# Optimization experiments

Measured on AMD Instinct MI355X. Metric: run time of the kernel, lower is better.

## Reference

```python
import jax, jax.numpy as jnp
import numpy as np

N_QUBITS = 12
K_STEPS = 6
VOCAB = 32000
D_EMB = 512
N_CLASSES = 8
B = 256
SEQ = 128
DIM = 2 ** N_QUBITS


def apply_1q(psi, U, q):
    # psi: [B, 2^n]; U: [2,2] (shared) or [B,2,2] (per-sample). Apply on wire q
    # (PennyLane convention: wire 0 = most significant axis).
    b = psi.shape[0]
    left, right = 2 ** q, 2 ** (N_QUBITS - q - 1)
    st = psi.reshape(b, left, 2, right)
    if U.ndim == 3:
        st = jnp.einsum('bij,bajr->bair', U, st)
    else:
        st = jnp.einsum('ij,bajr->bair', U, st)
    return st.reshape(b, DIM)


def apply_cnot(psi, c, t):
    b = psi.shape[0]
    st = psi.reshape((b,) + (2,) * N_QUBITS)
    c_ax, t_ax = 1 + c, 1 + t
    c0 = jnp.take(st, 0, axis=c_ax)
    c1 = jnp.take(st, 1, axis=c_ax)
    t_ax2 = t_ax - 1 if t_ax > c_ax else t_ax  # axis shift after take
    c1 = jnp.flip(c1, axis=t_ax2)
    return jnp.stack([c0, c1], axis=c_ax).reshape(b, DIM)


def ry_mat(angle):
    # angle: [B] -> [B,2,2] complex64
    c = jnp.cos(angle / 2)
    s = jnp.sin(angle / 2)
    row0 = jnp.stack([c, -s], axis=-1)
    row1 = jnp.stack([s, c], axis=-1)
    return jnp.stack([row0, row1], axis=-2).astype(jnp.complex64)


def rot_mat(phi, theta, omega):
    # PennyLane Rot(phi, theta, omega) = RZ(omega) RY(theta) RZ(phi)
    c = jnp.cos(theta / 2)
    s = jnp.sin(theta / 2)
    ep = jnp.exp(-0.5j * (phi + omega).astype(jnp.complex64))
    em = jnp.exp(0.5j * (phi - omega).astype(jnp.complex64))
    m = jnp.stack([jnp.stack([ep * c, -em * s]), jnp.stack([jnp.conj(em) * s, jnp.conj(ep) * c])])
    return m.astype(jnp.complex64)


def block(psi, x, theta_k):
    # data reupload RY(x_i), trainable Rot, ring of CNOTs (noiseless)
    for i in range(N_QUBITS):
        psi = apply_1q(psi, ry_mat(x[:, i]), i)
    for i in range(N_QUBITS):
        psi = apply_1q(psi, rot_mat(theta_k[i, 0], theta_k[i, 1], theta_k[i, 2]), i)
    for i in range(N_QUBITS - 1):
        psi = apply_cnot(psi, i, i + 1)
    psi = apply_cnot(psi, N_QUBITS - 1, 0)
    return psi


def z_expvals(psi):
    # <Z_i> for all wires from |psi|^2
    b = psi.shape[0]
    p = (psi.real ** 2 + psi.imag ** 2).reshape((b,) + (2,) * N_QUBITS)
    zs = []
    for i in range(N_QUBITS):
        axes = tuple(ax for ax in range(1, N_QUBITS + 1) if ax != 1 + i)
        m = p.sum(axis=axes)  # [B,2]
        zs.append(m[:, 0] - m[:, 1])
    return jnp.stack(zs, axis=-1)  # [B, n_qubits]


def _forward(input_ids, attention_mask, emb_table, proj_w, proj_b, theta, head_w, head_b):
    # encoder: embed -> masked mean pool -> tanh(linear) * pi
    e = emb_table[input_ids]                              # [B,S,D]
    mask = attention_mask[:, :, None].astype(jnp.float32)
    pooled = (e * mask).sum(axis=1) / jnp.clip(mask.sum(axis=1), 1.0)
    x = jnp.tanh(pooled @ proj_w.T + proj_b) * jnp.float32(np.pi)  # [B, n_qubits]

    b = x.shape[0]
    psi = jnp.zeros((b, DIM), jnp.complex64).at[:, 0].set(1.0)
    readouts = []
    for k in range(K_STEPS):
        psi = block(psi, x, theta[k])
        readouts.append(z_expvals(psi))
    step_readouts = jnp.stack(readouts, axis=0)           # [K,B,n_qubits]
    step_logits = step_readouts @ head_w.T + head_b       # [K,B,n_classes]
    return step_logits, step_readouts, step_logits[-1]


def setup_inputs() -> dict:
    key = jax.random.key(0)
    ks = jax.random.split(key, 6)
    input_ids = jax.random.randint(ks[0], (B, SEQ), 0, VOCAB)
    attention_mask = jnp.ones((B, SEQ), dtype=jnp.int32)
    emb_table = jax.random.normal(ks[1], (VOCAB, D_EMB), jnp.float32)
    emb_table = emb_table.at[0].set(0.0)  # padding_idx=0 row is zeros
    proj_w = jax.random.normal(ks[2], (N_QUBITS, D_EMB), jnp.float32) / np.sqrt(D_EMB)
    proj_b = jnp.zeros((N_QUBITS,), jnp.float32)
    theta = 0.01 * jax.random.normal(ks[3], (K_STEPS, N_QUBITS, 3), jnp.float32)
    head_w = jax.random.normal(ks[4], (N_CLASSES, N_QUBITS), jnp.float32) / np.sqrt(N_QUBITS)
    head_b = jnp.zeros((N_CLASSES,), jnp.float32)
    return {'input_ids': input_ids, 'attention_mask': attention_mask,
            'emb_table': emb_table, 'proj_w': proj_w, 'proj_b': proj_b,
            'theta': theta, 'head_w': head_w, 'head_b': head_b}


def reference(input_ids, attention_mask, emb_table, proj_w, proj_b, theta, head_w, head_b):
    return _forward(input_ids, attention_mask, emb_table, proj_w, proj_b, theta, head_w, head_b)
```

## Files before the change

### kernel.cpp

```cpp
#include <hip/hip_runtime.h>
#include <math.h>

#define NQ 12
#define DIM 4096
#define KS 6
#define BB 256
#define SEQ 128
#define DEMB 512


#define REG_GATE(P, W) { \
    const float* u = &s_u[k][W][0]; \
    float u00r=u[0],u00i=u[1],u01r=u[2],u01i=u[3]; \
    float u10r=u[4],u10i=u[5],u11r=u[6],u11i=u[7]; \
    _Pragma("unroll") \
    for (int r0 = 0; r0 < 8; ++r0) if (!(r0 & (1 << (P)))) { \
        int r1 = r0 | (1 << (P)); \
        float2 A = a[r0], Bv = a[r1]; \
        a[r0].x = u00r*A.x - u00i*A.y + u01r*Bv.x - u01i*Bv.y; \
        a[r0].y = u00r*A.y + u00i*A.x + u01r*Bv.y + u01i*Bv.x; \
        a[r1].x = u10r*A.x - u10i*A.y + u11r*Bv.x - u11i*Bv.y; \
        a[r1].y = u10r*A.y + u10i*A.x + u11r*Bv.y + u11i*Bv.x; \
    } }

#define BF_PLAIN(v, m) { float p_ = __shfl_xor(v, m, 64); v = v + p_; }
#define BF_SIGN(v, m)  { float p_ = __shfl_xor(v, m, 64); float d_ = v - p_; \
                         v = (lane & m) ? -d_ : d_; }

__global__ __launch_bounds__(512) void fused_kernel(
    const int* __restrict__ ids, const int* __restrict__ mask,
    const float* __restrict__ emb, const float* __restrict__ pw,
    const float* __restrict__ pb, const float* __restrict__ theta,
    const float* __restrict__ hw, const float* __restrict__ hb,
    float* __restrict__ readouts, float* __restrict__ logits,
    float* __restrict__ last)
{
    __shared__ float2 buf0[DIM];
    __shared__ float2 buf1[DIM];
    __shared__ float  s_u[KS][NQ][8];
    __shared__ float  s_red[8][NQ];
    __shared__ float  s_msum[4];
    __shared__ float  s_wred[2][NQ];
    __shared__ float  s_x[NQ];
    __shared__ float  s_hw[8 * NQ];
    __shared__ float  s_hb[8];

    int b = blockIdx.x;
    int tid = threadIdx.x;
    int lane = tid & 63, wave = tid >> 6;

    int*    s_ids = (int*)buf1;
    float*  s_m   = (float*)buf1 + SEQ;
    float4* s_part = (float4*)buf0;

    if (tid < SEQ) {
        s_ids[tid] = ids[b * SEQ + tid];
        s_m[tid]   = (float)mask[b * SEQ + tid];
    }
    if (tid >= 256 && tid < 256 + 8 * NQ) s_hw[tid - 256] = hw[tid - 256];
    if (tid >= 384 && tid < 392)          s_hb[tid - 384] = hb[tid - 384];
    __syncthreads();

    {
        int g = tid >> 7, e = tid & 127;
        float4 acc = make_float4(0.f, 0.f, 0.f, 0.f);
        float msum = 0.f;
        #pragma unroll 4
        for (int s = g; s < SEQ; s += 4) {
            float m = s_m[s];
            float4 v = ((const float4*)emb)[(size_t)s_ids[s] * 128 + e];
            acc.x = fmaf(m, v.x, acc.x);
            acc.y = fmaf(m, v.y, acc.y);
            acc.z = fmaf(m, v.z, acc.z);
            acc.w = fmaf(m, v.w, acc.w);
            msum += m;
        }
        __syncthreads();
        s_part[g * 128 + e] = acc;
        if (e == 0) s_msum[g] = msum;
    }
    __syncthreads();

    if (tid < 128) {
        float tm = fmaxf(s_msum[0] + s_msum[1] + s_msum[2] + s_msum[3], 1.f);
        float inv = 1.f / tm;
        float4 p0 = s_part[0 * 128 + tid], p1 = s_part[1 * 128 + tid];
        float4 p2 = s_part[2 * 128 + tid], p3 = s_part[3 * 128 + tid];
        float4 p;
        p.x = (p0.x + p1.x + p2.x + p3.x) * inv;
        p.y = (p0.y + p1.y + p2.y + p3.y) * inv;
        p.z = (p0.z + p1.z + p2.z + p3.z) * inv;
        p.w = (p0.w + p1.w + p2.w + p3.w) * inv;
        float z[NQ];
        #pragma unroll
        for (int i = 0; i < NQ; ++i) {
            float4 w4 = ((const float4*)pw)[i * 128 + tid];
            z[i] = p.x * w4.x + p.y * w4.y + p.z * w4.z + p.w * w4.w;
        }
        #pragma unroll
        for (int i = 0; i < NQ; ++i) {
            #pragma unroll
            for (int off = 32; off > 0; off >>= 1)
                z[i] += __shfl_xor(z[i], off, 64);
        }
        if ((tid & 63) == 0) {
            int w = tid >> 6;
            #pragma unroll
            for (int i = 0; i < NQ; ++i) s_wred[w][i] = z[i];
        }
    }
    __syncthreads();
    if (tid < NQ) {
        float d = pb[tid] + s_wred[0][tid] + s_wred[1][tid];
        s_x[tid] = tanhf(d) * 3.14159274101257324f;
    }
    __syncthreads();

    if (tid < KS * NQ) {
        int k = tid / NQ, w = tid % NQ;
        float ang = s_x[w];
        float cy = cosf(0.5f * ang), sy = sinf(0.5f * ang);
        const float* th = theta + (k * NQ + w) * 3;
        float phi = th[0], te = th[1], om = th[2];
        float ct = cosf(0.5f * te), st = sinf(0.5f * te);
        float a1 = -0.5f * (phi + om);
        float epr = cosf(a1), epi = sinf(a1);
        float a2 = 0.5f * (phi - om);
        float emr = cosf(a2), emi = sinf(a2);
        float R00r = epr * ct,  R00i = epi * ct;
        float R01r = -emr * st, R01i = -emi * st;
        float R10r = emr * st,  R10i = -emi * st;
        float R11r = epr * ct,  R11i = -epi * ct;
        s_u[k][w][0] =  R00r * cy + R01r * sy;
        s_u[k][w][1] =  R00i * cy + R01i * sy;
        s_u[k][w][2] = -R00r * sy + R01r * cy;
        s_u[k][w][3] = -R00i * sy + R01i * cy;
        s_u[k][w][4] =  R10r * cy + R11r * sy;
        s_u[k][w][5] =  R10i * cy + R11i * sy;
        s_u[k][w][6] = -R10r * sy + R11r * cy;
        s_u[k][w][7] = -R10i * sy + R11i * cy;
    }

    int baseWA = (tid << 3) ^ ((tid >> 1) & 15);
    int baseRB = ((lane << 3) | wave) ^ ((lane >> 1) & 15);
    int idxP[8];
    #pragma unroll
    for (int rb = 0; rb < 8; ++rb) {
        int jp = (rb << 9) | (lane << 3) | wave;
        int b0 = (jp >> 11) & 1;
        int pref = b0, outv = 0;
        for (int w = 1; w < NQ; ++w) {
            pref ^= (jp >> (11 - w)) & 1;
            outv |= pref << (11 - w);
        }
        outv |= (b0 ^ pref) << 11;
        idxP[rb] = outv ^ ((outv >> 4) & 15);
    }
    int wv2 = (wave >> 2) & 1, wv21 = ((wave >> 2) ^ (wave >> 1)) & 1;
    int wvp = ((wave >> 2) ^ (wave >> 1) ^ wave) & 1;

    float2 a[8];
    #pragma unroll
    for (int r = 0; r < 8; ++r) a[r] = make_float2(0.f, 0.f);
    if (tid == 0) a[0].x = 1.f;
    __syncthreads();

    for (int k = 0; k < KS; ++k) {
        REG_GATE(0, 11)
        REG_GATE(1, 10)
        REG_GATE(2, 9)

        #pragma unroll
        for (int p = 3; p <= 8; ++p) {
            const float* u = &s_u[k][11 - p][0];
            int q = p - 3, mk = 1 << q;
            int bit = (lane >> q) & 1;
            float c0r = bit ? u[6] : u[0];
            float c0i = bit ? u[7] : u[1];
            float c1r = bit ? u[4] : u[2];
            float c1i = bit ? u[5] : u[3];
            #pragma unroll
            for (int r = 0; r < 8; ++r) {
                float px = __shfl_xor(a[r].x, mk, 64);
                float py = __shfl_xor(a[r].y, mk, 64);
                float nx = c0r * a[r].x - c0i * a[r].y + c1r * px - c1i * py;
                float ny = c0r * a[r].y + c0i * a[r].x + c1r * py + c1i * px;
                a[r].x = nx; a[r].y = ny;
            }
        }

        #pragma unroll
        for (int r = 0; r < 8; ++r) buf0[baseWA ^ r] = a[r];
        __syncthreads();
        #pragma unroll
        for (int rb = 0; rb < 8; ++rb) a[rb] = buf0[(rb << 9) | baseRB];

        REG_GATE(0, 2)
        REG_GATE(1, 1)
        REG_GATE(2, 0)

        float pr[8];
        #pragma unroll
        for (int r = 0; r < 8; ++r)
            pr[r] = a[r].x * a[r].x + a[r].y * a[r].y;
        float r1 = (pr[0] + pr[1] + pr[6] + pr[7]) - (pr[2] + pr[3] + pr[4] + pr[5]);
        float D  = (pr[0] + pr[3] + pr[5] + pr[6]) - (pr[1] + pr[2] + pr[4] + pr[7]);
        float D0 = (pr[0] + pr[3] + pr[4] + pr[7]) - (pr[1] + pr[2] + pr[5] + pr[6]);
        float r2 = D, r3 = D, r4 = D, r5 = D, r6 = D, r7 = D, r8 = D, r0 = D0;
        BF_PLAIN(r1,32) BF_PLAIN(r2,32) BF_SIGN(r3,32) BF_SIGN(r4,32)
        BF_SIGN(r5,32)  BF_SIGN(r6,32)  BF_SIGN(r7,32) BF_SIGN(r8,32) BF_SIGN(r0,32)
        BF_PLAIN(r1,16) BF_PLAIN(r2,16) BF_PLAIN(r3,16) BF_SIGN(r4,16)
        BF_SIGN(r5,16)  BF_SIGN(r6,16)  BF_SIGN(r7,16) BF_SIGN(r8,16) BF_SIGN(r0,16)
        BF_PLAIN(r1,8)  BF_PLAIN(r2,8)  BF_PLAIN(r3,8) BF_PLAIN(r4,8)
        BF_SIGN(r5,8)   BF_SIGN(r6,8)   BF_SIGN(r7,8)  BF_SIGN(r8,8)  BF_SIGN(r0,8)
        BF_PLAIN(r1,4)  BF_PLAIN(r2,4)  BF_PLAIN(r3,4) BF_PLAIN(r4,4)
        BF_PLAIN(r5,4)  BF_SIGN(r6,4)   BF_SIGN(r7,4)  BF_SIGN(r8,4)  BF_SIGN(r0,4)
        BF_PLAIN(r1,2)  BF_PLAIN(r2,2)  BF_PLAIN(r3,2) BF_PLAIN(r4,2)
        BF_PLAIN(r5,2)  BF_PLAIN(r6,2)  BF_SIGN(r7,2)  BF_SIGN(r8,2)  BF_SIGN(r0,2)
        BF_PLAIN(r1,1)  BF_PLAIN(r2,1)  BF_PLAIN(r3,1) BF_PLAIN(r4,1)
        BF_PLAIN(r5,1)  BF_PLAIN(r6,1)  BF_PLAIN(r7,1) BF_SIGN(r8,1)  BF_SIGN(r0,1)
        if (lane == 0) {
            float* sr = s_red[wave];
            sr[0]  = wvp  ? -r0 : r0;
            sr[1]  = r1;  sr[2] = r2;  sr[3] = r3;  sr[4] = r4;
            sr[5]  = r5;  sr[6] = r6;  sr[7] = r7;  sr[8] = r8;
            sr[9]  = wv2  ? -r8 : r8;
            sr[10] = wv21 ? -r8 : r8;
            sr[11] = wvp  ? -r8 : r8;
        }

        #pragma unroll
        for (int rb = 0; rb < 8; ++rb) buf1[idxP[rb]] = a[rb];
        __syncthreads();
        #pragma unroll
        for (int r = 0; r < 8; ++r) a[r] = buf1[baseWA ^ r];

        if (tid < NQ) {
            float s = 0.f;
            #pragma unroll
            for (int w2 = 0; w2 < 8; ++w2) s += s_red[w2][tid];
            readouts[(k * BB + b) * NQ + tid] = s;
        }
        if (tid < 8) {
            float acc2 = s_hb[tid];
            #pragma unroll
            for (int i = 0; i < NQ; ++i) {
                float si = 0.f;
                #pragma unroll
                for (int w2 = 0; w2 < 8; ++w2) si += s_red[w2][i];
                acc2 = fmaf(si, s_hw[tid * NQ + i], acc2);
            }
            logits[(k * BB + b) * 8 + tid] = acc2;
            if (k == KS - 1) last[b * 8 + tid] = acc2;
        }
    }
}

extern "C" void kernel_launch(void* const* d_in, const int* in_sizes, int n_in,
                              void* d_out, int out_size, void* d_ws, size_t ws_size,
                              hipStream_t stream) {
    const int*   ids   = (const int*)d_in[0];
    const int*   mask  = (const int*)d_in[1];
    const float* emb   = (const float*)d_in[2];
    const float* pw    = (const float*)d_in[3];
    const float* pb    = (const float*)d_in[4];
    const float* theta = (const float*)d_in[5];
    const float* hw    = (const float*)d_in[6];
    const float* hb    = (const float*)d_in[7];
    float* out = (float*)d_out;

    float* readouts = out + KS * BB * 8;
    float* last     = out + KS * BB * 8 + KS * BB * NQ;

    fused_kernel<<<BB, 512, 0, stream>>>(ids, mask, emb, pw, pb, theta,
                                         hw, hb, readouts, out, last);
}
```

Measured before the change: 141.7 us.

## Double threads per block to 1024 with four amplitudes per thread

Each block now runs 1024 threads that each hold 4 complex amplitudes instead of 8, and the qubit-to-register/lane/wave mapping, LDS transpose indices, CNOT permutation and Z-expectation butterfly reductions are rederived for 16 waves. The embedding gather is split across 8 sequence groups, with partial sums stored in both shared buffers. The aim is more parallelism and less register pressure per thread for the 256 blocks. In exchange there are more shuffle-based gates, a 16-way cross-wave reduction, and barriers now span more waves.

Measured after the change: 153.1 us. +8.0%, slower.

```diff
diff --git a/kernel.cpp b/kernel.cpp
--- a/kernel.cpp
+++ b/kernel.cpp
@@ -14,7 +14,7 @@
     float u00r=u[0],u00i=u[1],u01r=u[2],u01i=u[3]; \
     float u10r=u[4],u10i=u[5],u11r=u[6],u11i=u[7]; \
     _Pragma("unroll") \
-    for (int r0 = 0; r0 < 8; ++r0) if (!(r0 & (1 << (P)))) { \
+    for (int r0 = 0; r0 < 4; ++r0) if (!(r0 & (1 << (P)))) { \
         int r1 = r0 | (1 << (P)); \
         float2 A = a[r0], Bv = a[r1]; \
         a[r0].x = u00r*A.x - u00i*A.y + u01r*Bv.x - u01i*Bv.y; \
@@ -27,7 +27,7 @@
 #define BF_SIGN(v, m)  { float p_ = __shfl_xor(v, m, 64); float d_ = v - p_; \
                          v = (lane & m) ? -d_ : d_; }
 
-__global__ __launch_bounds__(512) void fused_kernel(
+__global__ __launch_bounds__(1024) void fused_kernel(
     const int* __restrict__ ids, const int* __restrict__ mask,
     const float* __restrict__ emb, const float* __restrict__ pw,
     const float* __restrict__ pb, const float* __restrict__ theta,
@@ -38,8 +38,8 @@
     __shared__ float2 buf0[DIM];
     __shared__ float2 buf1[DIM];
     __shared__ float  s_u[KS][NQ][8];
-    __shared__ float  s_red[8][NQ];
-    __shared__ float  s_msum[4];
+    __shared__ float  s_red[16][NQ];
+    __shared__ float  s_msum[8];
     __shared__ float  s_wred[2][NQ];
     __shared__ float  s_x[NQ];
     __shared__ float  s_hw[8 * NQ];
@@ -49,9 +49,8 @@
     int tid = threadIdx.x;
     int lane = tid & 63, wave = tid >> 6;
 
-    int*    s_ids = (int*)buf1;
-    float*  s_m   = (float*)buf1 + SEQ;
-    float4* s_part = (float4*)buf0;
+    int*   s_ids = (int*)buf1;
+    float* s_m   = (float*)buf1 + SEQ;
 
     if (tid < SEQ) {
         s_ids[tid] = ids[b * SEQ + tid];
@@ -66,7 +65,7 @@
         float4 acc = make_float4(0.f, 0.f, 0.f, 0.f);
         float msum = 0.f;
         #pragma unroll 4
-        for (int s = g; s < SEQ; s += 4) {
+        for (int s = g; s < SEQ; s += 8) {
             float m = s_m[s];
             float4 v = ((const float4*)emb)[(size_t)s_ids[s] * 128 + e];
             acc.x = fmaf(m, v.x, acc.x);
@@ -76,21 +75,26 @@
             msum += m;
         }
         __syncthreads();
-        s_part[g * 128 + e] = acc;
+        float4* part = (g & 4) ? (float4*)buf1 : (float4*)buf0;
+        part[(g & 3) * 128 + e] = acc;
         if (e == 0) s_msum[g] = msum;
     }
     __syncthreads();
 
     if (tid < 128) {
-        float tm = fmaxf(s_msum[0] + s_msum[1] + s_msum[2] + s_msum[3], 1.f);
-        float inv = 1.f / tm;
-        float4 p0 = s_part[0 * 128 + tid], p1 = s_part[1 * 128 + tid];
-        float4 p2 = s_part[2 * 128 + tid], p3 = s_part[3 * 128 + tid];
-        float4 p;
-        p.x = (p0.x + p1.x + p2.x + p3.x) * inv;
-        p.y = (p0.y + p1.y + p2.y + p3.y) * inv;
-        p.z = (p0.z + p1.z + p2.z + p3.z) * inv;
-        p.w = (p0.w + p1.w + p2.w + p3.w) * inv;
+        float tm = 0.f;
+        #pragma unroll
+        for (int i = 0; i < 8; ++i) tm += s_msum[i];
+        float inv = 1.f / fmaxf(tm, 1.f);
+        float4 p = make_float4(0.f, 0.f, 0.f, 0.f);
+        #pragma unroll
+        for (int i = 0; i < 4; ++i) {
+            float4 q0 = ((float4*)buf0)[i * 128 + tid];
+            float4 q1 = ((float4*)buf1)[i * 128 + tid];
+            p.x += q0.x + q1.x; p.y += q0.y + q1.y;
+            p.z += q0.z + q1.z; p.w += q0.w + q1.w;
+        }
+        p.x *= inv; p.y *= inv; p.z *= inv; p.w *= inv;
         float z[NQ];
         #pragma unroll
         for (int i = 0; i < NQ; ++i) {
@@ -141,12 +145,14 @@
         s_u[k][w][7] = -R10i * sy + R11i * cy;
     }
 
-    int baseWA = (tid << 3) ^ ((tid >> 1) & 15);
-    int baseRB = ((lane << 3) | wave) ^ ((lane >> 1) & 15);
-    int idxP[8];
+    int baseWA = (tid << 2) ^ ((tid >> 2) & 15);
+    int jB0 = ((lane & 3) << 10) | (((lane >> 2) & 15) << 2)
+            | ((wave & 3) << 6) | ((wave >> 2) & 3);
+    int baseRB = jB0 ^ (((lane >> 4) & 3) | ((wave & 3) << 2));
+    int idxP[4];
     #pragma unroll
-    for (int rb = 0; rb < 8; ++rb) {
-        int jp = (rb << 9) | (lane << 3) | wave;
+    for (int rq = 0; rq < 4; ++rq) {
+        int jp = jB0 | (rq << 8);
         int b0 = (jp >> 11) & 1;
         int pref = b0, outv = 0;
         for (int w = 1; w < NQ; ++w) {
@@ -154,33 +160,33 @@
             outv |= pref << (11 - w);
         }
         outv |= (b0 ^ pref) << 11;
-        idxP[rb] = outv ^ ((outv >> 4) & 15);
-    }
-    int wv2 = (wave >> 2) & 1, wv21 = ((wave >> 2) ^ (wave >> 1)) & 1;
-    int wvp = ((wave >> 2) ^ (wave >> 1) ^ wave) & 1;
-
-    float2 a[8];
+        idxP[rq] = outv ^ ((outv >> 4) & 15);
+    }
+    int w0b = wave & 1, w1b = (wave >> 1) & 1;
+    int w2b = (wave >> 2) & 1, w3b = (wave >> 3) & 1;
+    int sW = w0b ^ w1b;
+
+    float2 a[4];
     #pragma unroll
-    for (int r = 0; r < 8; ++r) a[r] = make_float2(0.f, 0.f);
+    for (int r = 0; r < 4; ++r) a[r] = make_float2(0.f, 0.f);
     if (tid == 0) a[0].x = 1.f;
     __syncthreads();
 
     for (int k = 0; k < KS; ++k) {
         REG_GATE(0, 11)
         REG_GATE(1, 10)
-        REG_GATE(2, 9)
-
-        #pragma unroll
-        for (int p = 3; p <= 8; ++p) {
-            const float* u = &s_u[k][11 - p][0];
-            int q = p - 3, mk = 1 << q;
+
+        #pragma unroll
+        for (int q = 0; q < 6; ++q) {
+            const float* u = &s_u[k][9 - q][0];
+            int mk = 1 << q;
             int bit = (lane >> q) & 1;
             float c0r = bit ? u[6] : u[0];
             float c0i = bit ? u[7] : u[1];
             float c1r = bit ? u[4] : u[2];
             float c1i = bit ? u[5] : u[3];
             #pragma unroll
-            for (int r = 0; r < 8; ++r) {
+            for (int r = 0; r < 4; ++r) {
                 float px = __shfl_xor(a[r].x, mk, 64);
                 float py = __shfl_xor(a[r].y, mk, 64);
                 float nx = c0r * a[r].x - c0i * a[r].y + c1r * px - c1i * py;
@@ -190,55 +196,80 @@
         }
 
         #pragma unroll
-        for (int r = 0; r < 8; ++r) buf0[baseWA ^ r] = a[r];
+        for (int r = 0; r < 4; ++r) buf0[baseWA ^ r] = a[r];
         __syncthreads();
         #pragma unroll
-        for (int rb = 0; rb < 8; ++rb) a[rb] = buf0[(rb << 9) | baseRB];
-
-        REG_GATE(0, 2)
-        REG_GATE(1, 1)
-        REG_GATE(2, 0)
-
-        float pr[8];
-        #pragma unroll
-        for (int r = 0; r < 8; ++r)
-            pr[r] = a[r].x * a[r].x + a[r].y * a[r].y;
-        float r1 = (pr[0] + pr[1] + pr[6] + pr[7]) - (pr[2] + pr[3] + pr[4] + pr[5]);
-        float D  = (pr[0] + pr[3] + pr[5] + pr[6]) - (pr[1] + pr[2] + pr[4] + pr[7]);
-        float D0 = (pr[0] + pr[3] + pr[4] + pr[7]) - (pr[1] + pr[2] + pr[5] + pr[6]);
-        float r2 = D, r3 = D, r4 = D, r5 = D, r6 = D, r7 = D, r8 = D, r0 = D0;
-        BF_PLAIN(r1,32) BF_PLAIN(r2,32) BF_SIGN(r3,32) BF_SIGN(r4,32)
-        BF_SIGN(r5,32)  BF_SIGN(r6,32)  BF_SIGN(r7,32) BF_SIGN(r8,32) BF_SIGN(r0,32)
-        BF_PLAIN(r1,16) BF_PLAIN(r2,16) BF_PLAIN(r3,16) BF_SIGN(r4,16)
-        BF_SIGN(r5,16)  BF_SIGN(r6,16)  BF_SIGN(r7,16) BF_SIGN(r8,16) BF_SIGN(r0,16)
-        BF_PLAIN(r1,8)  BF_PLAIN(r2,8)  BF_PLAIN(r3,8) BF_PLAIN(r4,8)
-        BF_SIGN(r5,8)   BF_SIGN(r6,8)   BF_SIGN(r7,8)  BF_SIGN(r8,8)  BF_SIGN(r0,8)
-        BF_PLAIN(r1,4)  BF_PLAIN(r2,4)  BF_PLAIN(r3,4) BF_PLAIN(r4,4)
-        BF_PLAIN(r5,4)  BF_SIGN(r6,4)   BF_SIGN(r7,4)  BF_SIGN(r8,4)  BF_SIGN(r0,4)
-        BF_PLAIN(r1,2)  BF_PLAIN(r2,2)  BF_PLAIN(r3,2) BF_PLAIN(r4,2)
-        BF_PLAIN(r5,2)  BF_PLAIN(r6,2)  BF_SIGN(r7,2)  BF_SIGN(r8,2)  BF_SIGN(r0,2)
-        BF_PLAIN(r1,1)  BF_PLAIN(r2,1)  BF_PLAIN(r3,1) BF_PLAIN(r4,1)
-        BF_PLAIN(r5,1)  BF_PLAIN(r6,1)  BF_PLAIN(r7,1) BF_SIGN(r8,1)  BF_SIGN(r0,1)
+        for (int rq = 0; rq < 4; ++rq) a[rq] = buf0[baseRB | (rq << 8)];
+
+        REG_GATE(0, 3)
+        REG_GATE(1, 2)
+
+        #pragma unroll
+        for (int q = 0; q < 2; ++q) {
+            const float* u = &s_u[k][1 - q][0];
+            int mk = 1 << q;
+            int bit = (lane >> q) & 1;
+            float c0r = bit ? u[6] : u[0];
+            float c0i = bit ? u[7] : u[1];
+            float c1r = bit ? u[4] : u[2];
+            float c1i = bit ? u[5] : u[3];
+            #pragma unroll
+            for (int r = 0; r < 4; ++r) {
+                float px = __shfl_xor(a[r].x, mk, 64);
+                float py = __shfl_xor(a[r].y, mk, 64);
+                float nx = c0r * a[r].x - c0i * a[r].y + c1r * px - c1i * py;
+                float ny = c0r * a[r].y + c0i * a[r].x + c1r * py + c1i * px;
+                a[r].x = nx; a[r].y = ny;
+            }
+        }
+
+        float pr0 = a[0].x*a[0].x + a[0].y*a[0].y;
+        float pr1 = a[1].x*a[1].x + a[1].y*a[1].y;
+        float pr2 = a[2].x*a[2].x + a[2].y*a[2].y;
+        float pr3 = a[3].x*a[3].x + a[3].y*a[3].y;
+        float T   = pr0 + pr1 + pr2 + pr3;
+        float P9  = (pr0 + pr1) - (pr2 + pr3);
+        float P98 = (pr0 + pr3) - (pr1 + pr2);
+        float v1 = T, v2 = P9, v3 = P98;
+        float v6 = P98, v7 = P98, v8 = P98, v9 = P98, v0 = P98;
+        BF_PLAIN(v1,32) BF_PLAIN(v2,32) BF_PLAIN(v3,32) BF_SIGN(v6,32)
+        BF_SIGN(v7,32)  BF_SIGN(v8,32)  BF_SIGN(v9,32)  BF_SIGN(v0,32)
+        BF_PLAIN(v1,16) BF_PLAIN(v2,16) BF_PLAIN(v3,16) BF_PLAIN(v6,16)
+        BF_SIGN(v7,16)  BF_SIGN(v8,16)  BF_SIGN(v9,16)  BF_SIGN(v0,16)
+        BF_PLAIN(v1,8)  BF_PLAIN(v2,8)  BF_PLAIN(v3,8)  BF_PLAIN(v6,8)
+        BF_PLAIN(v7,8)  BF_SIGN(v8,8)   BF_SIGN(v9,8)   BF_SIGN(v0,8)
+        BF_PLAIN(v1,4)  BF_PLAIN(v2,4)  BF_PLAIN(v3,4)  BF_PLAIN(v6,4)
+        BF_PLAIN(v7,4)  BF_PLAIN(v8,4)  BF_SIGN(v9,4)   BF_SIGN(v0,4)
+        BF_SIGN(v1,2)   BF_SIGN(v2,2)   BF_SIGN(v3,2)   BF_SIGN(v6,2)
+        BF_SIGN(v7,2)   BF_SIGN(v8,2)   BF_SIGN(v9,2)   BF_PLAIN(v0,2)
+        BF_SIGN(v1,1)   BF_SIGN(v2,1)   BF_SIGN(v3,1)   BF_SIGN(v6,1)
+        BF_SIGN(v7,1)   BF_SIGN(v8,1)   BF_SIGN(v9,1)   BF_SIGN(v0,1)
         if (lane == 0) {
             float* sr = s_red[wave];
-            sr[0]  = wvp  ? -r0 : r0;
-            sr[1]  = r1;  sr[2] = r2;  sr[3] = r3;  sr[4] = r4;
-            sr[5]  = r5;  sr[6] = r6;  sr[7] = r7;  sr[8] = r8;
-            sr[9]  = wv2  ? -r8 : r8;
-            sr[10] = wv21 ? -r8 : r8;
-            sr[11] = wvp  ? -r8 : r8;
-        }
-
-        #pragma unroll
-        for (int rb = 0; rb < 8; ++rb) buf1[idxP[rb]] = a[rb];
+            sr[0]  = ((w0b^w1b^w2b^w3b) ? -v0 : v0);
+            sr[1]  = v1;
+            sr[2]  = v2;
+            sr[3]  = v3;
+            sr[4]  = w1b ? -v3 : v3;
+            sr[5]  = sW  ? -v3 : v3;
+            sr[6]  = sW  ? -v6 : v6;
+            sr[7]  = sW  ? -v7 : v7;
+            sr[8]  = sW  ? -v8 : v8;
+            sr[9]  = sW  ? -v9 : v9;
+            sr[10] = ((sW^w3b) ? -v9 : v9);
+            sr[11] = ((sW^w3b^w2b) ? -v9 : v9);
+        }
+
+        #pragma unroll
+        for (int rq = 0; rq < 4; ++rq) buf1[idxP[rq]] = a[rq];
         __syncthreads();
         #pragma unroll
-        for (int r = 0; r < 8; ++r) a[r] = buf1[baseWA ^ r];
+        for (int r = 0; r < 4; ++r) a[r] = buf1[baseWA ^ r];
 
         if (tid < NQ) {
             float s = 0.f;
             #pragma unroll
-            for (int w2 = 0; w2 < 8; ++w2) s += s_red[w2][tid];
+            for (int w2 = 0; w2 < 16; ++w2) s += s_red[w2][tid];
             readouts[(k * BB + b) * NQ + tid] = s;
         }
         if (tid < 8) {
@@ -247,7 +278,7 @@
             for (int i = 0; i < NQ; ++i) {
                 float si = 0.f;
                 #pragma unroll
-                for (int w2 = 0; w2 < 8; ++w2) si += s_red[w2][i];
+                for (int w2 = 0; w2 < 16; ++w2) si += s_red[w2][i];
                 acc2 = fmaf(si, s_hw[tid * NQ + i], acc2);
             }
             logits[(k * BB + b) * 8 + tid] = acc2;
@@ -272,6 +303,6 @@
     float* readouts = out + KS * BB * 8;
     float* last     = out + KS * BB * 8 + KS * BB * NQ;
 
-    fused_kernel<<<BB, 512, 0, stream>>>(ids, mask, emb, pw, pb, theta,
-                                         hw, hb, readouts, out, last);
+    fused_kernel<<<BB, 1024, 0, stream>>>(ids, mask, emb, pw, pb, theta,
+                                          hw, hb, readouts, out, last);
 }
```

## Replace shuffle-based middle gates with LDS transposes and restructure Z reduction

Applied to the files above, without the earlier changes.

The six middle-wire gates per step were applied with cross-lane shuffles, two per amplitude per gate. They now go through two extra shared-memory transposes, so every gate acts on register-resident pairs. The swizzle is changed to allow float4 stores and loads on the contiguous transpose, and the Z-expectation butterfly is rebuilt as a cascade that shares partial sums. This trades many shuffles for two extra barriers and more LDS traffic per step.

Measured after the change: 140.2 us. No clear change (-1.1%).

```diff
diff --git a/kernel.cpp b/kernel.cpp
--- a/kernel.cpp
+++ b/kernel.cpp
@@ -27,6 +27,8 @@
 #define BF_SIGN(v, m)  { float p_ = __shfl_xor(v, m, 64); float d_ = v - p_; \
                          v = (lane & m) ? -d_ : d_; }
 
+__device__ __forceinline__ int swz14(int x) { return x ^ ((x >> 4) & 14); }
+
 __global__ __launch_bounds__(512) void fused_kernel(
     const int* __restrict__ ids, const int* __restrict__ mask,
     const float* __restrict__ emb, const float* __restrict__ pw,
@@ -35,8 +37,8 @@
     float* __restrict__ readouts, float* __restrict__ logits,
     float* __restrict__ last)
 {
-    __shared__ float2 buf0[DIM];
-    __shared__ float2 buf1[DIM];
+    __shared__ __align__(16) float2 buf0[DIM];
+    __shared__ __align__(16) float2 buf1[DIM];
     __shared__ float  s_u[KS][NQ][8];
     __shared__ float  s_red[8][NQ];
     __shared__ float  s_msum[4];
@@ -49,8 +51,8 @@
     int tid = threadIdx.x;
     int lane = tid & 63, wave = tid >> 6;
 
-    int*    s_ids = (int*)buf1;
-    float*  s_m   = (float*)buf1 + SEQ;
+    int*   s_ids = (int*)buf1;
+    float* s_m   = (float*)buf1 + SEQ;
     float4* s_part = (float4*)buf0;
 
     if (tid < SEQ) {
@@ -141,23 +143,27 @@
         s_u[k][w][7] = -R10i * sy + R11i * cy;
     }
 
-    int baseWA = (tid << 3) ^ ((tid >> 1) & 15);
-    int baseRB = ((lane << 3) | wave) ^ ((lane >> 1) & 15);
-    int idxP[8];
+    int T8 = tid << 3;
+    int baseA  = swz14(T8);
+    int baseA4 = baseA >> 1;
+    int addrB[8], addrC[8], addrD[8], idxP[8];
     #pragma unroll
-    for (int rb = 0; rb < 8; ++rb) {
-        int jp = (rb << 9) | (lane << 3) | wave;
-        int b0 = (jp >> 11) & 1;
+    for (int r = 0; r < 8; ++r) {
+        addrB[r] = swz14((lane & 7) + 8 * r + 64 * (lane >> 3) + 512 * wave);
+        addrC[r] = swz14(lane + 64 * r + 512 * wave);
+        int jD   = lane + 64 * wave + 512 * r;
+        addrD[r] = swz14(jD);
+        int b0 = (jD >> 11) & 1;
         int pref = b0, outv = 0;
         for (int w = 1; w < NQ; ++w) {
-            pref ^= (jp >> (11 - w)) & 1;
+            pref ^= (jD >> (11 - w)) & 1;
             outv |= pref << (11 - w);
         }
         outv |= (b0 ^ pref) << 11;
-        idxP[rb] = outv ^ ((outv >> 4) & 15);
-    }
-    int wv2 = (wave >> 2) & 1, wv21 = ((wave >> 2) ^ (wave >> 1)) & 1;
-    int wvp = ((wave >> 2) ^ (wave >> 1) ^ wave) & 1;
+        idxP[r] = swz14(outv);
+    }
+    int w0b = wave & 1, w1b = (wave >> 1) & 1, w2b = (wave >> 2) & 1;
+    int wall = w0b ^ w1b ^ w2b;
 
     float2 a[8];
     #pragma unroll
@@ -166,74 +172,89 @@
     __syncthreads();
 
     for (int k = 0; k < KS; ++k) {
-        REG_GATE(0, 11)
-        REG_GATE(1, 10)
-        REG_GATE(2, 9)
-
-        #pragma unroll
-        for (int p = 3; p <= 8; ++p) {
-            const float* u = &s_u[k][11 - p][0];
-            int q = p - 3, mk = 1 << q;
-            int bit = (lane >> q) & 1;
-            float c0r = bit ? u[6] : u[0];
-            float c0i = bit ? u[7] : u[1];
-            float c1r = bit ? u[4] : u[2];
-            float c1i = bit ? u[5] : u[3];
-            #pragma unroll
-            for (int r = 0; r < 8; ++r) {
-                float px = __shfl_xor(a[r].x, mk, 64);
-                float py = __shfl_xor(a[r].y, mk, 64);
-                float nx = c0r * a[r].x - c0i * a[r].y + c1r * px - c1i * py;
-                float ny = c0r * a[r].y + c0i * a[r].x + c1r * py + c1i * px;
-                a[r].x = nx; a[r].y = ny;
+        REG_GATE(0, 11) REG_GATE(1, 10) REG_GATE(2, 9)
+
+        #pragma unroll
+        for (int i = 0; i < 4; ++i)
+            ((float4*)buf0)[baseA4 ^ i] =
+                make_float4(a[2*i].x, a[2*i].y, a[2*i+1].x, a[2*i+1].y);
+        __syncthreads();
+        #pragma unroll
+        for (int r = 0; r < 8; ++r) a[r] = buf0[addrB[r]];
+
+        REG_GATE(0, 8) REG_GATE(1, 7) REG_GATE(2, 6)
+
+        #pragma unroll
+        for (int r = 0; r < 8; ++r) buf1[addrB[r]] = a[r];
+        __syncthreads();
+        #pragma unroll
+        for (int r = 0; r < 8; ++r) a[r] = buf1[addrC[r]];
+
+        REG_GATE(0, 5) REG_GATE(1, 4) REG_GATE(2, 3)
+
+        #pragma unroll
+        for (int r = 0; r < 8; ++r) buf0[addrC[r]] = a[r];
+        __syncthreads();
+        #pragma unroll
+        for (int r = 0; r < 8; ++r) a[r] = buf0[addrD[r]];
+
+        REG_GATE(0, 2) REG_GATE(1, 1) REG_GATE(2, 0)
+
+        {
+            float p[8];
+            #pragma unroll
+            for (int r = 0; r < 8; ++r)
+                p[r] = a[r].x * a[r].x + a[r].y * a[r].y;
+            float Q1 = (p[0]+p[1]+p[6]+p[7]) - (p[2]+p[3]+p[4]+p[5]);
+            float Q2 = (p[0]+p[3]+p[5]+p[6]) - (p[1]+p[2]+p[4]+p[7]);
+            float Q0 = (p[0]+p[3]+p[4]+p[7]) - (p[1]+p[2]+p[5]+p[6]);
+            float q1 = Q1, q2p = Q2, q0 = Q0;
+            BF_PLAIN(q1,32) BF_PLAIN(q1,16) BF_PLAIN(q1,8)
+            BF_PLAIN(q1,4)  BF_PLAIN(q1,2)  BF_PLAIN(q1,1)
+            BF_PLAIN(q2p,32) BF_PLAIN(q2p,16) BF_PLAIN(q2p,8)
+            BF_PLAIN(q2p,4)  BF_PLAIN(q2p,2)  BF_PLAIN(q2p,1)
+            BF_SIGN(q0,32) BF_SIGN(q0,16) BF_SIGN(q0,8)
+            BF_SIGN(q0,4)  BF_SIGN(q0,2)  BF_SIGN(q0,1)
+            float c = Q2;
+            BF_SIGN(c,32);
+            float w6v = c; BF_PLAIN(w6v,16) BF_PLAIN(w6v,8) BF_PLAIN(w6v,4)
+                           BF_PLAIN(w6v,2)  BF_PLAIN(w6v,1)
+            BF_SIGN(c,16);
+            float w7v = c; BF_PLAIN(w7v,8) BF_PLAIN(w7v,4)
+                           BF_PLAIN(w7v,2) BF_PLAIN(w7v,1)
+            BF_SIGN(c,8);
+            float w8v = c; BF_PLAIN(w8v,4) BF_PLAIN(w8v,2) BF_PLAIN(w8v,1)
+            BF_SIGN(c,4);
+            float w9v = c; BF_PLAIN(w9v,2) BF_PLAIN(w9v,1)
+            BF_SIGN(c,2);
+            float w10v = c; BF_PLAIN(w10v,1)
+            BF_SIGN(c,1);
+            if (lane == 0) {
+                float* sr = s_red[wave];
+                sr[0]  = wall ? -q0  : q0;
+                sr[1]  = q1;
+                sr[2]  = q2p;
+                sr[3]  = w2b ? -q2p : q2p;
+                sr[4]  = (w1b ^ w2b) ? -q2p : q2p;
+                sr[5]  = wall ? -q2p : q2p;
+                sr[6]  = wall ? -w6v : w6v;
+                sr[7]  = wall ? -w7v : w7v;
+                sr[8]  = wall ? -w8v : w8v;
+                sr[9]  = wall ? -w9v : w9v;
+                sr[10] = wall ? -w10v : w10v;
+                sr[11] = wall ? -c   : c;
             }
         }
 
         #pragma unroll
-        for (int r = 0; r < 8; ++r) buf0[baseWA ^ r] = a[r];
-        __syncthreads();
-        #pragma unroll
-        for (int rb = 0; rb < 8; ++rb) a[rb] = buf0[(rb << 9) | baseRB];
-
-        REG_GATE(0, 2)
-        REG_GATE(1, 1)
-        REG_GATE(2, 0)
-
-        float pr[8];
-        #pragma unroll
-        for (int r = 0; r < 8; ++r)
-            pr[r] = a[r].x * a[r].x + a[r].y * a[r].y;
-        float r1 = (pr[0] + pr[1] + pr[6] + pr[7]) - (pr[2] + pr[3] + pr[4] + pr[5]);
-        float D  = (pr[0] + pr[3] + pr[5] + pr[6]) - (pr[1] + pr[2] + pr[4] + pr[7]);
-        float D0 = (pr[0] + pr[3] + pr[4] + pr[7]) - (pr[1] + pr[2] + pr[5] + pr[6]);
-        float r2 = D, r3 = D, r4 = D, r5 = D, r6 = D, r7 = D, r8 = D, r0 = D0;
-        BF_PLAIN(r1,32) BF_PLAIN(r2,32) BF_SIGN(r3,32) BF_SIGN(r4,32)
-        BF_SIGN(r5,32)  BF_SIGN(r6,32)  BF_SIGN(r7,32) BF_SIGN(r8,32) BF_SIGN(r0,32)
-        BF_PLAIN(r1,16) BF_PLAIN(r2,16) BF_PLAIN(r3,16) BF_SIGN(r4,16)
-        BF_SIGN(r5,16)  BF_SIGN(r6,16)  BF_SIGN(r7,16) BF_SIGN(r8,16) BF_SIGN(r0,16)
-        BF_PLAIN(r1,8)  BF_PLAIN(r2,8)  BF_PLAIN(r3,8) BF_PLAIN(r4,8)
-        BF_SIGN(r5,8)   BF_SIGN(r6,8)   BF_SIGN(r7,8)  BF_SIGN(r8,8)  BF_SIGN(r0,8)
-        BF_PLAIN(r1,4)  BF_PLAIN(r2,4)  BF_PLAIN(r3,4) BF_PLAIN(r4,4)
-        BF_PLAIN(r5,4)  BF_SIGN(r6,4)   BF_SIGN(r7,4)  BF_SIGN(r8,4)  BF_SIGN(r0,4)
-        BF_PLAIN(r1,2)  BF_PLAIN(r2,2)  BF_PLAIN(r3,2) BF_PLAIN(r4,2)
-        BF_PLAIN(r5,2)  BF_PLAIN(r6,2)  BF_SIGN(r7,2)  BF_SIGN(r8,2)  BF_SIGN(r0,2)
-        BF_PLAIN(r1,1)  BF_PLAIN(r2,1)  BF_PLAIN(r3,1) BF_PLAIN(r4,1)
-        BF_PLAIN(r5,1)  BF_PLAIN(r6,1)  BF_PLAIN(r7,1) BF_SIGN(r8,1)  BF_SIGN(r0,1)
-        if (lane == 0) {
-            float* sr = s_red[wave];
-            sr[0]  = wvp  ? -r0 : r0;
-            sr[1]  = r1;  sr[2] = r2;  sr[3] = r3;  sr[4] = r4;
-            sr[5]  = r5;  sr[6] = r6;  sr[7] = r7;  sr[8] = r8;
-            sr[9]  = wv2  ? -r8 : r8;
-            sr[10] = wv21 ? -r8 : r8;
-            sr[11] = wvp  ? -r8 : r8;
-        }
-
-        #pragma unroll
-        for (int rb = 0; rb < 8; ++rb) buf1[idxP[rb]] = a[rb];
-        __syncthreads();
-        #pragma unroll
-        for (int r = 0; r < 8; ++r) a[r] = buf1[baseWA ^ r];
+        for (int r = 0; r < 8; ++r) buf1[idxP[r]] = a[r];
+        __syncthreads();
+        #pragma unroll
+        for (int i = 0; i < 4; ++i) {
+            float4 v = ((float4*)buf1)[baseA4 ^ i];
+            a[2*i]   = make_float2(v.x, v.y);
+            a[2*i+1] = make_float2(v.z, v.w);
+        }
 
         if (tid < NQ) {
             float s = 0.f;
```
